# Optimization experiments

Measured on AMD Instinct MI355X. Metric: run time of the kernel, lower is better.

## Reference

```python
import jax, jax.numpy as jnp
import numpy as np

B, L, H, NH, DH = 2, 4096, 768, 12, 64
W_ = 128          # one-sided sliding window
NL = 2            # encoder layers
VOCAB, OUT, FF = 50265, 384, 3072
EPS = 1e-5


def _ln(x, s, b):
    m = jnp.mean(x, axis=-1, keepdims=True)
    v = jnp.mean((x - m) ** 2, axis=-1, keepdims=True)
    return (x - m) / jnp.sqrt(v + EPS) * s + b


def _attn(x, amask, Wq, bq, Wk, bk, Wv, bv, Wo, bo):
    # x: [B,L,H]; sliding-window attention (one-sided W_) + global token 0
    def heads(Wt, bt):
        return (x @ Wt + bt).reshape(B, L, NH, DH).transpose(0, 2, 1, 3)  # [B,NH,L,DH]
    q, k, v = heads(Wq, bq), heads(Wk, bk), heads(Wv, bv)
    scale = 1.0 / np.sqrt(DH).astype(np.float32)
    C = W_
    nC = L // C
    qc = q.reshape(B, NH, nC, C, DH)

    def blocks(t):  # gather [prev, self, next] key chunks -> [B,NH,nC,3C,DH]
        tc = t.reshape(B, NH, nC, C, DH)
        tp = jnp.pad(tc, ((0, 0), (0, 0), (1, 1), (0, 0), (0, 0)))
        return jnp.concatenate([tp[:, :, :-2], tp[:, :, 1:-1], tp[:, :, 2:]], axis=3)

    k3, v3 = blocks(k), blocks(v)
    s_loc = jnp.einsum('bhncd,bhnkd->bhnck', qc, k3) * scale  # [B,NH,nC,C,3C]

    pos_k = (jnp.arange(nC)[:, None] - 1) * C + jnp.arange(3 * C)[None, :]  # [nC,3C]
    pos_q = jnp.arange(nC)[:, None] * C + jnp.arange(C)[None, :]            # [nC,C]
    within = jnp.abs(pos_q[:, :, None] - pos_k[:, None, :]) <= W_           # [nC,C,3C]
    valid = (pos_k >= 0) & (pos_k < L) & (pos_k != 0)  # key 0 handled as global column
    mk = amask[:, jnp.clip(pos_k, 0, L - 1)] > 0        # [B,nC,3C]
    m = within[None, None] & valid[None, None, :, None, :] & mk[:, None, :, None, :]
    s_loc = jnp.where(m, s_loc, -1e9)

    # every token also attends to the global token 0
    s_g = jnp.einsum('bhld,bhd->bhl', q, k[:, :, 0]) * scale  # [B,NH,L]
    s = jnp.concatenate([s_loc.reshape(B, NH, L, 3 * C), s_g[..., None]], axis=-1)
    p = jax.nn.softmax(s, axis=-1)
    p_loc = p[..., :3 * C].reshape(B, NH, nC, C, 3 * C)
    out = jnp.einsum('bhnck,bhnkd->bhncd', p_loc, v3).reshape(B, NH, L, DH)
    out = out + p[..., -1:] * v[:, :, 0][:, :, None, :]

    # global token 0 attends to everything
    s0 = jnp.einsum('bhd,bhld->bhl', q[:, :, 0], k) * scale
    s0 = jnp.where(amask[:, None, :] > 0, s0, -1e9)
    o0 = jnp.einsum('bhl,bhld->bhd', jax.nn.softmax(s0, axis=-1), v)
    out = out.at[:, :, 0, :].set(o0)

    out = out.transpose(0, 2, 1, 3).reshape(B, L, H)
    return out @ Wo + bo


def setup_inputs() -> dict:
    key = jax.random.key(0)
    ks = jax.random.split(key, 16)
    p = lambda k_, sh: 0.02 * jax.random.normal(k_, sh, jnp.float32)
    return {
        'input_ids': jax.random.randint(ks[0], (B, L), 0, VOCAB, dtype=jnp.int32),
        'attention_mask': jnp.ones((B, L), jnp.int32),
        'word_emb': p(ks[1], (VOCAB, H)),
        'pos_emb': p(ks[2], (L, H)),
        'emb_ln_s': jnp.ones((H,), jnp.float32), 'emb_ln_b': jnp.zeros((H,), jnp.float32),
        'Wq': p(ks[3], (NL, H, H)), 'bq': jnp.zeros((NL, H), jnp.float32),
        'Wk': p(ks[4], (NL, H, H)), 'bk': jnp.zeros((NL, H), jnp.float32),
        'Wv': p(ks[5], (NL, H, H)), 'bv': jnp.zeros((NL, H), jnp.float32),
        'Wo': p(ks[6], (NL, H, H)), 'bo': jnp.zeros((NL, H), jnp.float32),
        'ln1_s': jnp.ones((NL, H), jnp.float32), 'ln1_b': jnp.zeros((NL, H), jnp.float32),
        'W1': p(ks[7], (NL, H, FF)), 'b1': jnp.zeros((NL, FF), jnp.float32),
        'W2': p(ks[8], (NL, FF, H)), 'b2': jnp.zeros((NL, H), jnp.float32),
        'ln2_s': jnp.ones((NL, H), jnp.float32), 'ln2_b': jnp.zeros((NL, H), jnp.float32),
        'Wfc': p(ks[9], (H, OUT)), 'bfc': jnp.zeros((OUT,), jnp.float32),
    }


def reference(input_ids, attention_mask, word_emb, pos_emb, emb_ln_s, emb_ln_b,
              Wq, bq, Wk, bk, Wv, bv, Wo, bo, ln1_s, ln1_b,
              W1, b1, W2, b2, ln2_s, ln2_b, Wfc, bfc):
    x = word_emb[input_ids] + pos_emb[None]
    x = _ln(x, emb_ln_s, emb_ln_b)
    for l in range(NL):
        a = _attn(x, attention_mask, Wq[l], bq[l], Wk[l], bk[l], Wv[l], bv[l], Wo[l], bo[l])
        x = _ln(x + a, ln1_s[l], ln1_b[l])
        h = jax.nn.gelu(x @ W1[l] + b1[l])
        x = _ln(x + h @ W2[l] + b2[l], ln2_s[l], ln2_b[l])
    v_dn = x @ Wfc + bfc           # [B,L,OUT]
    cls = v_dn[:, 0]               # fc(last_hidden[:,0]) == v_dn[:,0]
    return v_dn, cls
```

## Files before the change

kernel.cpp:

```cpp
#include <hip/hip_runtime.h>
#include <hip/hip_bf16.h>
#include <stdint.h>

#define L_SEQ 4096
#define H_DIM 768
#define N_HEADS 12
#define D_HEAD 64
#define N_CHUNK 32
#define CHUNK 128
#define FF_DIM 3072
#define OUT_DIM 384
#define BATCH 2
#define EPS_LN 1e-5f
#define M_ROWS (BATCH * L_SEQ)
#define QKV_LD (3 * H_DIM)
#define NSEG 16

typedef unsigned short u16;
typedef __bf16 bx8 __attribute__((ext_vector_type(8)));
typedef float fx4 __attribute__((ext_vector_type(4)));
typedef u16 ux8 __attribute__((ext_vector_type(8)));

__device__ __forceinline__ u16 f2bf(float f) {
  union { float f; unsigned u; } x; x.f = f;
  unsigned r = x.u + 0x7fffu + ((x.u >> 16) & 1u);
  return (u16)(r >> 16);
}
__device__ __forceinline__ float bf2f(u16 v) {
  union { unsigned u; float f; } x; x.u = ((unsigned)v) << 16;
  return x.f;
}

__device__ __forceinline__ void gload16(const void* g, void* l) {
  __builtin_amdgcn_global_load_lds((const __attribute__((address_space(1))) void*)g,
                                   (__attribute__((address_space(3))) void*)l, 16, 0, 0);
}

template<int OUT_BF16, int DO_GELU, int DO_CLS>
__global__ __launch_bounds__(256, 3)
void gemm_s(const u16* __restrict__ A, const u16* __restrict__ Bt,
            const float* __restrict__ bias,
            float* __restrict__ Cf, u16* __restrict__ Cb,
            float* __restrict__ cls,
            int N, int K)
{
  __shared__ __align__(16) u16 As[128 * 64];
  __shared__ __align__(16) u16 Bs[128 * 64];
  const int tid = threadIdx.x;
  const int lane = tid & 63, w = tid >> 6;
  const int c16 = lane & 15, g = lane >> 4;
  const int wr = w >> 1, wc = w & 1;

  const int nbn = N >> 7;
  int id = blockIdx.x;
  id = (id & 7) * (gridDim.x >> 3) + (id >> 3);
  const int bm = id / nbn, bn = id % nbn;

  const int srow = w * 8 + (lane >> 3);
  const int schunk = (lane & 7) ^ (lane >> 3);
  const u16* sA = A + (size_t)(bm * 128 + srow) * K + schunk * 8;
  const u16* sB = Bt + (size_t)(bn * 128 + srow) * K + schunk * 8;
  const int wdst = w * 512;

  fx4 acc[4][4] = {};

  for (int k0 = 0; k0 < K; k0 += 64) {
    #pragma unroll
    for (int i = 0; i < 4; i++) {
      gload16(sA + (size_t)(i * 32) * K + k0, &As[i * 2048 + wdst]);
      gload16(sB + (size_t)(i * 32) * K + k0, &Bs[i * 2048 + wdst]);
    }
    __syncthreads();
    #pragma unroll
    for (int h = 0; h < 2; h++) {
      bx8 af[4], bf[4];
      #pragma unroll
      for (int m = 0; m < 4; m++) {
        const int row = wr * 64 + m * 16 + c16;
        af[m] = *(const bx8*)&As[row * 64 + (((h << 2) + g) ^ (c16 & 7)) * 8];
      }
      #pragma unroll
      for (int n = 0; n < 4; n++) {
        const int row = wc * 64 + n * 16 + c16;
        bf[n] = *(const bx8*)&Bs[row * 64 + (((h << 2) + g) ^ (c16 & 7)) * 8];
      }
      #pragma unroll
      for (int m = 0; m < 4; m++)
        #pragma unroll
        for (int n = 0; n < 4; n++)
          acc[m][n] = __builtin_amdgcn_mfma_f32_16x16x32_bf16(af[m], bf[n], acc[m][n], 0, 0, 0);
    }
    __syncthreads();
  }

  const int row0 = bm * 128 + wr * 64 + g * 4;
  const int col0 = bn * 128 + wc * 64 + c16;
  #pragma unroll
  for (int n = 0; n < 4; n++) {
    const int col = col0 + n * 16;
    const float bb = bias[col];
    #pragma unroll
    for (int m = 0; m < 4; m++) {
      #pragma unroll
      for (int r = 0; r < 4; r++) {
        float y = acc[m][n][r] + bb;
        if (DO_GELU) {
          const float tt = y;
          y = 0.5f * tt * (1.0f + tanhf(0.7978845608f * (tt + 0.044715f * tt * tt * tt)));
        }
        const int row = row0 + m * 16 + r;
        const size_t idx = (size_t)row * N + col;
        if (OUT_BF16) Cb[idx] = f2bf(y);
        else Cf[idx] = y;
        if (DO_CLS) {
          if ((row & (L_SEQ - 1)) == 0)
            cls[(row >> 12) * OUT_DIM + col] = y;
        }
      }
    }
  }
}

#define KV_W 384
#define P_STR 128

__global__ __launch_bounds__(512, 2)
void attn_local_kernel(const u16* __restrict__ qkv, const int* __restrict__ amask,
                       u16* __restrict__ attnout)
{
  __shared__ __align__(16) u16 Klds[KV_W * 64];
  __shared__ __align__(16) u16 Vlds[64 * KV_W];
  __shared__ __align__(16) u16 Plds[8 * 16 * P_STR];

  const int tid = threadIdx.x;
  const int lane = tid & 63, w = tid >> 6;
  const int c16 = lane & 15, g = lane >> 4;

  const int bh = blockIdx.x >> 5;
  const int n = blockIdx.x & 31;
  const int b = bh / N_HEADS, h = bh % N_HEADS;

  const u16* qkvb = qkv + (size_t)b * L_SEQ * QKV_LD + h * D_HEAD;
  const int chunk_lo = n * CHUNK - CHUNK;

  #pragma unroll
  for (int it = 0; it < 6; it++) {
    const int row = it * 64 + w * 8 + (lane >> 3);
    const int sc = (lane & 7) ^ (row & 7);
    int pos = chunk_lo + row;
    if (pos < 0) pos = 0;
    if (pos >= L_SEQ) pos = L_SEQ - 1;
    gload16(qkvb + (size_t)pos * QKV_LD + H_DIM + sc * 8,
            &Klds[it * 4096 + w * 512]);
  }

  {
    const int d = lane;
    #pragma unroll
    for (int it = 0; it < 6; it++) {
      const int kb = it * 8 + w;
      ux8 vals;
      #pragma unroll
      for (int j = 0; j < 8; j++) {
        int pos = chunk_lo + kb * 8 + j;
        if (pos < 0) pos = 0;
        if (pos >= L_SEQ) pos = L_SEQ - 1;
        vals[j] = qkvb[(size_t)pos * QKV_LD + 2 * H_DIM + d];
      }
      *(ux8*)&Vlds[d * KV_W + ((kb ^ (d & 7)) << 3)] = vals;
    }
  }

  const int qrow = n * CHUNK + w * 16 + c16;
  const u16* qp = qkvb + (size_t)qrow * QKV_LD + g * 8;
  const bx8 aq0 = *(const bx8*)qp;
  const bx8 aq1 = *(const bx8*)(qp + 32);

  unsigned kvm = 0;
  #pragma unroll
  for (int kf = 0; kf < 24; kf++) {
    const int pos = chunk_lo + kf * 16 + c16;
    bool ok = (pos >= 1) && (pos < L_SEQ);
    if (ok) ok = (amask[b * L_SEQ + pos] > 0);
    kvm |= ((unsigned)ok) << kf;
  }

  const int cq = w * 16 + g * 4;

  float m[4], l[4], pgv[4];
  {
    const u16* kp = qkvb + H_DIM + g * 8;
    const bx8 b0 = *(const bx8*)kp;
    const bx8 b1 = *(const bx8*)(kp + 32);
    fx4 sg = {};
    sg = __builtin_amdgcn_mfma_f32_16x16x32_bf16(aq0, b0, sg, 0, 0, 0);
    sg = __builtin_amdgcn_mfma_f32_16x16x32_bf16(aq1, b1, sg, 0, 0, 0);
    #pragma unroll
    for (int r = 0; r < 4; r++) {
      const float val = (c16 == 0) ? sg[r] * 0.125f : -1.0e9f;
      float mm = val;
      mm = fmaxf(mm, __shfl_xor(mm, 1));
      mm = fmaxf(mm, __shfl_xor(mm, 2));
      mm = fmaxf(mm, __shfl_xor(mm, 4));
      mm = fmaxf(mm, __shfl_xor(mm, 8));
      m[r] = mm;
      pgv[r] = __expf(val - mm);
      float t = pgv[r];
      t += __shfl_xor(t, 1);
      t += __shfl_xor(t, 2);
      t += __shfl_xor(t, 4);
      t += __shfl_xor(t, 8);
      l[r] = t;
    }
  }

  __syncthreads();

  fx4 o[4] = {};
  u16* pb = Plds + w * 16 * P_STR;
  const int prow = (w * 16 + c16) * P_STR;

  #pragma unroll
  for (int pass = 0; pass < 4; pass++) {
    fx4 s[6];
    #pragma unroll
    for (int kf6 = 0; kf6 < 6; kf6++) {
      const int kf = pass * 6 + kf6;
      const int krow = kf * 16 + c16;
      const bx8 b0 = *(const bx8*)&Klds[krow * 64 + ((g ^ (c16 & 7)) << 3)];
      const bx8 b1 = *(const bx8*)&Klds[krow * 64 + (((4 + g) ^ (c16 & 7)) << 3)];
      fx4 a = {};
      a = __builtin_amdgcn_mfma_f32_16x16x32_bf16(aq0, b0, a, 0, 0, 0);
      a = __builtin_amdgcn_mfma_f32_16x16x32_bf16(aq1, b1, a, 0, 0, 0);
      s[kf6] = a;
    }
    float pmax[4];
    #pragma unroll
    for (int r = 0; r < 4; r++) pmax[r] = -3.0e38f;
    #pragma unroll
    for (int kf6 = 0; kf6 < 6; kf6++) {
      const int kf = pass * 6 + kf6;
      const int j = kf * 16 + c16;
      const bool kv = ((kvm >> kf) & 1u) != 0;
      #pragma unroll
      for (int r = 0; r < 4; r++) {
        const int c = cq + r;
        const bool keep = kv && (j >= c && j <= c + 256);
        const float val = keep ? s[kf6][r] * 0.125f : -1.0e9f;
        s[kf6][r] = val;
        pmax[r] = fmaxf(pmax[r], val);
      }
    }
    #pragma unroll
    for (int r = 0; r < 4; r++) {
      float mm = pmax[r];
      mm = fmaxf(mm, __shfl_xor(mm, 1));
      mm = fmaxf(mm, __shfl_xor(mm, 2));
      mm = fmaxf(mm, __shfl_xor(mm, 4));
      mm = fmaxf(mm, __shfl_xor(mm, 8));
      const float newm = fmaxf(m[r], mm);
      const float scale = __expf(m[r] - newm);
      m[r] = newm;
      l[r] *= scale;
      pgv[r] *= scale;
      #pragma unroll
      for (int df = 0; df < 4; df++) o[df][r] *= scale;
    }
    float lsum[4] = {0.f, 0.f, 0.f, 0.f};
    #pragma unroll
    for (int kf6 = 0; kf6 < 6; kf6++)
      #pragma unroll
      for (int r = 0; r < 4; r++) {
        const float p = __expf(s[kf6][r] - m[r]);
        s[kf6][r] = p;
        lsum[r] += p;
      }
    #pragma unroll
    for (int r = 0; r < 4; r++) {
      float t = lsum[r];
      t += __shfl_xor(t, 1);
      t += __shfl_xor(t, 2);
      t += __shfl_xor(t, 4);
      t += __shfl_xor(t, 8);
      l[r] += t;
    }
    #pragma unroll
    for (int kf6 = 0; kf6 < 6; kf6++) {
      #pragma unroll
      for (int r = 0; r < 4; r++) {
        const int rr = g * 4 + r;
        const int jj = kf6 * 16 + c16;
        pb[rr * P_STR + (((jj >> 3) ^ (rr & 7)) << 3) + (jj & 7)] = f2bf(s[kf6][r]);
      }
    }
    #pragma unroll
    for (int t = 0; t < 3; t++) {
      const int ckp = t * 4 + g;
      const bx8 pa = *(const bx8*)&Plds[prow + ((ckp ^ (c16 & 7)) << 3)];
      const int ckv = pass * 12 + ckp;
      #pragma unroll
      for (int df = 0; df < 4; df++) {
        const int vrow = df * 16 + c16;
        const bx8 vvf = *(const bx8*)&Vlds[vrow * KV_W + ((ckv ^ (c16 & 7)) << 3)];
        o[df] = __builtin_amdgcn_mfma_f32_16x16x32_bf16(pa, vvf, o[df], 0, 0, 0);
      }
    }
  }

  float rinv[4], pg[4];
  #pragma unroll
  for (int r = 0; r < 4; r++) {
    rinv[r] = 1.0f / l[r];
    pg[r] = __shfl(pgv[r], g * 16);
  }
  u16* ob = attnout + (size_t)b * L_SEQ * H_DIM + h * D_HEAD;
  const int posq = n * CHUNK + w * 16 + g * 4;
  #pragma unroll
  for (int df = 0; df < 4; df++) {
    const float v0f = bf2f(qkvb[2 * H_DIM + df * 16 + c16]);
    #pragma unroll
    for (int r = 0; r < 4; r++)
      ob[(size_t)(posq + r) * H_DIM + df * 16 + c16] =
          f2bf((o[df][r] + pg[r] * v0f) * rinv[r]);
  }
}

__global__ __launch_bounds__(256)
void attn_g_score(const u16* __restrict__ qkv, const int* __restrict__ amask,
                  float* __restrict__ sbuf, float* __restrict__ pmax)
{
  __shared__ float qs[D_HEAD];
  __shared__ float red[4];
  const int seg = blockIdx.x, bh = blockIdx.y;
  const int b = bh / N_HEADS, h = bh % N_HEADS;
  const u16* base = qkv + (size_t)b * L_SEQ * QKV_LD + h * D_HEAD;
  const int tid = threadIdx.x;

  if (tid < D_HEAD) qs[tid] = bf2f(base[tid]);
  __syncthreads();

  const int l = seg * 256 + tid;
  const ux8* kp = (const ux8*)(base + (size_t)l * QKV_LD + H_DIM);
  float dot = 0.f;
  #pragma unroll
  for (int i = 0; i < 8; i++) {
    const ux8 kv = kp[i];
    #pragma unroll
    for (int j = 0; j < 8; j++) dot += qs[i * 8 + j] * bf2f(kv[j]);
  }
  float sv = dot * 0.125f;
  if (amask[b * L_SEQ + l] == 0) sv = -1.0e9f;
  sbuf[(size_t)bh * L_SEQ + l] = sv;

  float m = sv;
  #pragma unroll
  for (int off = 32; off > 0; off >>= 1) m = fmaxf(m, __shfl_xor(m, off));
  if ((tid & 63) == 0) red[tid >> 6] = m;
  __syncthreads();
  if (tid == 0)
    pmax[bh * NSEG + seg] = fmaxf(fmaxf(red[0], red[1]), fmaxf(red[2], red[3]));
}

__global__ __launch_bounds__(256)
void attn_g_pv(const u16* __restrict__ qkv, const float* __restrict__ sbuf,
               const float* __restrict__ pmax, float* __restrict__ psum,
               float* __restrict__ po)
{
  __shared__ float es[256];
  __shared__ float red[4];
  const int seg = blockIdx.x, bh = blockIdx.y;
  const int b = bh / N_HEADS, h = bh % N_HEADS;
  const int tid = threadIdx.x;

  float M = -3.0e38f;
  #pragma unroll
  for (int i = 0; i < NSEG; i++) M = fmaxf(M, pmax[bh * NSEG + i]);

  const int l = seg * 256 + tid;
  const float e = __expf(sbuf[(size_t)bh * L_SEQ + l] - M);
  es[tid] = e;

  float t = e;
  #pragma unroll
  for (int off = 32; off > 0; off >>= 1) t += __shfl_xor(t, off);
  if ((tid & 63) == 0) red[tid >> 6] = t;
  __syncthreads();
  if (tid == 0) psum[bh * NSEG + seg] = red[0] + red[1] + red[2] + red[3];

  const int d = tid & 63, grp = tid >> 6;
  const u16* vb = qkv + (size_t)b * L_SEQ * QKV_LD + h * D_HEAD + 2 * H_DIM + d;
  float acc = 0.f;
  #pragma unroll 4
  for (int i = 0; i < 64; i++) {
    const int ll = seg * 256 + grp * 64 + i;
    acc += es[grp * 64 + i] * bf2f(vb[(size_t)ll * QKV_LD]);
  }
  po[(((size_t)bh * NSEG + seg) * 4 + grp) * D_HEAD + d] = acc;
}

__global__ __launch_bounds__(64)
void attn_g_combine(const float* __restrict__ psum, const float* __restrict__ po,
                    u16* __restrict__ attnout)
{
  const int bh = blockIdx.x;
  const int b = bh / N_HEADS, h = bh % N_HEADS;
  const int d = threadIdx.x;
  float S = 0.f;
  #pragma unroll
  for (int i = 0; i < NSEG; i++) S += psum[bh * NSEG + i];
  float acc = 0.f;
  #pragma unroll
  for (int i = 0; i < NSEG * 4; i++)
    acc += po[((size_t)bh * NSEG * 4 + i) * D_HEAD + d];
  attnout[(size_t)b * L_SEQ * H_DIM + h * D_HEAD + d] = f2bf(acc / S);
}

__device__ __forceinline__ void block_stats(float sum, float sq, float* red,
                                            float& mean, float& rstd)
{
  const int lane = threadIdx.x & 63, wv = threadIdx.x >> 6;
  #pragma unroll
  for (int off = 32; off > 0; off >>= 1) {
    sum += __shfl_xor(sum, off);
    sq  += __shfl_xor(sq, off);
  }
  if (lane == 0) { red[wv] = sum; red[4 + wv] = sq; }
  __syncthreads();
  sum = red[0] + red[1] + red[2] + red[3];
  sq  = red[4] + red[5] + red[6] + red[7];
  mean = sum * (1.0f / H_DIM);
  const float var = sq * (1.0f / H_DIM) - mean * mean;
  rstd = rsqrtf(var + EPS_LN);
}

__global__ __launch_bounds__(256)
void embed_ln_kernel(const int* __restrict__ ids, const float* __restrict__ wemb,
                     const float* __restrict__ pemb, const float* __restrict__ gam,
                     const float* __restrict__ bet, u16* __restrict__ xb)
{
  __shared__ float red[8];
  const int row = blockIdx.x, tid = threadIdx.x;
  const int l = row & (L_SEQ - 1);
  const int id = ids[row];
  float v[3]; float sum = 0.f, sq = 0.f;
  #pragma unroll
  for (int i = 0; i < 3; i++) {
    const int c = tid + i * 256;
    const float t = wemb[(size_t)id * H_DIM + c] + pemb[(size_t)l * H_DIM + c];
    v[i] = t; sum += t; sq += t * t;
  }
  float mean, rstd;
  block_stats(sum, sq, red, mean, rstd);
  #pragma unroll
  for (int i = 0; i < 3; i++) {
    const int c = tid + i * 256;
    const float y = (v[i] - mean) * rstd * gam[c] + bet[c];
    xb[(size_t)row * H_DIM + c] = f2bf(y);
  }
}

__global__ __launch_bounds__(256)
void add_ln_kernel(u16* xio, const u16* __restrict__ yin,
                   const float* __restrict__ gam, const float* __restrict__ bet)
{
  __shared__ float red[8];
  const int row = blockIdx.x, tid = threadIdx.x;
  float v[3]; float sum = 0.f, sq = 0.f;
  #pragma unroll
  for (int i = 0; i < 3; i++) {
    const int c = tid + i * 256;
    const float t = bf2f(xio[(size_t)row * H_DIM + c]) + bf2f(yin[(size_t)row * H_DIM + c]);
    v[i] = t; sum += t; sq += t * t;
  }
  float mean, rstd;
  block_stats(sum, sq, red, mean, rstd);
  #pragma unroll
  for (int i = 0; i < 3; i++) {
    const int c = tid + i * 256;
    const float y = (v[i] - mean) * rstd * gam[c] + bet[c];
    xio[(size_t)row * H_DIM + c] = f2bf(y);
  }
}

__global__ __launch_bounds__(256)
void prep_weights(const float* __restrict__ Wq, const float* __restrict__ Wk,
                  const float* __restrict__ Wv, const float* __restrict__ Wo,
                  const float* __restrict__ W1, const float* __restrict__ W2,
                  const float* __restrict__ Wfc,
                  const float* __restrict__ bq, const float* __restrict__ bk,
                  const float* __restrict__ bv,
                  u16* __restrict__ wqkvT, u16* __restrict__ woT,
                  u16* __restrict__ w1T, u16* __restrict__ w2T,
                  u16* __restrict__ wfcT, float* __restrict__ bqkv)
{
  const int t = blockIdx.x;
  const int tid = threadIdx.x;
  if (t >= 14112) {
    const int idx = t - 14112;
    const int l = idx / 9, j = idx % 9;
    const int i = j * 256 + tid;
    if (i < H_DIM)          bqkv[l * QKV_LD + i] = bq[l * H_DIM + i];
    else if (i < 2 * H_DIM) bqkv[l * QKV_LD + i] = bk[l * H_DIM + i - H_DIM];
    else if (i < 3 * H_DIM) bqkv[l * QKV_LD + i] = bv[l * H_DIM + i - 2 * H_DIM];
    return;
  }
  const float* src; u16* dst; int K, N, r;
  if (t < 13824) {
    const int l = t / 6912; r = t % 6912;
    if (r < 2304) {
      const int m = r / 576; r = r % 576; K = H_DIM; N = H_DIM;
      if (m == 0)      src = Wq + (size_t)l * H_DIM * H_DIM;
      else if (m == 1) src = Wk + (size_t)l * H_DIM * H_DIM;
      else if (m == 2) src = Wv + (size_t)l * H_DIM * H_DIM;
      else             src = Wo + (size_t)l * H_DIM * H_DIM;
      dst = (m < 3) ? wqkvT + (size_t)l * QKV_LD * H_DIM + (size_t)m * H_DIM * H_DIM
                    : woT + (size_t)l * H_DIM * H_DIM;
    } else if (r < 4608) {
      r -= 2304; K = H_DIM; N = FF_DIM;
      src = W1 + (size_t)l * H_DIM * FF_DIM;
      dst = w1T + (size_t)l * FF_DIM * H_DIM;
    } else {
      r -= 4608; K = FF_DIM; N = H_DIM;
      src = W2 + (size_t)l * FF_DIM * H_DIM;
      dst = w2T + (size_t)l * H_DIM * FF_DIM;
    }
  } else {
    r = t - 13824; K = H_DIM; N = OUT_DIM; src = Wfc; dst = wfcT;
  }
  const int ntn = N >> 5;
  const int k0 = (r / ntn) * 32, n0 = (r % ntn) * 32;
  __shared__ float tile[32][33];
  const int tx = tid & 31, ty = tid >> 5;
  #pragma unroll
  for (int i = 0; i < 32; i += 8)
    tile[ty + i][tx] = src[(size_t)(k0 + ty + i) * N + n0 + tx];
  __syncthreads();
  #pragma unroll
  for (int i = 0; i < 32; i += 8)
    dst[(size_t)(n0 + ty + i) * K + k0 + tx] = f2bf(tile[tx][ty + i]);
}

extern "C" void kernel_launch(void* const* d_in, const int* in_sizes, int n_in,
                              void* d_out, int out_size, void* d_ws, size_t ws_size,
                              hipStream_t stream)
{
  (void)in_sizes; (void)n_in; (void)out_size; (void)ws_size;
  const int*   ids   = (const int*)d_in[0];
  const int*   amask = (const int*)d_in[1];
  const float* wemb  = (const float*)d_in[2];
  const float* pemb  = (const float*)d_in[3];
  const float* elns  = (const float*)d_in[4];
  const float* elnb  = (const float*)d_in[5];
  const float* Wq    = (const float*)d_in[6];
  const float* bq    = (const float*)d_in[7];
  const float* Wk    = (const float*)d_in[8];
  const float* bk    = (const float*)d_in[9];
  const float* Wv    = (const float*)d_in[10];
  const float* bv    = (const float*)d_in[11];
  const float* Wo    = (const float*)d_in[12];
  const float* bo    = (const float*)d_in[13];
  const float* ln1s  = (const float*)d_in[14];
  const float* ln1b  = (const float*)d_in[15];
  const float* W1    = (const float*)d_in[16];
  const float* b1    = (const float*)d_in[17];
  const float* W2    = (const float*)d_in[18];
  const float* b2    = (const float*)d_in[19];
  const float* ln2s  = (const float*)d_in[20];
  const float* ln2b  = (const float*)d_in[21];
  const float* Wfc   = (const float*)d_in[22];
  const float* bfc   = (const float*)d_in[23];

  char* ws = (char*)d_ws;
  size_t off = 0;
  auto alloc = [&](size_t bytes) -> void* {
    void* p = ws + off;
    off += (bytes + 255) & ~(size_t)255;
    return p;
  };
  u16* xb     = (u16*)alloc((size_t)M_ROWS * H_DIM * 2);
  u16* projb  = (u16*)alloc((size_t)M_ROWS * H_DIM * 2);
  u16* big    = (u16*)alloc((size_t)M_ROWS * FF_DIM * 2);
  u16* attno  = (u16*)alloc((size_t)M_ROWS * H_DIM * 2);
  u16* wqkvT  = (u16*)alloc((size_t)2 * QKV_LD * H_DIM * 2);
  u16* woT    = (u16*)alloc((size_t)2 * H_DIM * H_DIM * 2);
  u16* w1T    = (u16*)alloc((size_t)2 * FF_DIM * H_DIM * 2);
  u16* w2T    = (u16*)alloc((size_t)2 * H_DIM * FF_DIM * 2);
  u16* wfcT   = (u16*)alloc((size_t)OUT_DIM * H_DIM * 2);
  float* bqkv = (float*)alloc(2 * QKV_LD * 4);
  float* gsc  = (float*)alloc((size_t)BATCH * N_HEADS * L_SEQ * 4);
  float* gpm  = (float*)alloc((size_t)BATCH * N_HEADS * NSEG * 4);
  float* gps  = (float*)alloc((size_t)BATCH * N_HEADS * NSEG * 4);
  float* gpo  = (float*)alloc((size_t)BATCH * N_HEADS * NSEG * 4 * D_HEAD * 4);

  u16* qkvb = big;
  u16* ff1  = big;

  prep_weights<<<14130, 256, 0, stream>>>(Wq, Wk, Wv, Wo, W1, W2, Wfc,
                                          bq, bk, bv,
                                          wqkvT, woT, w1T, w2T, wfcT, bqkv);
  embed_ln_kernel<<<M_ROWS, 256, 0, stream>>>(ids, wemb, pemb, elns, elnb, xb);

  for (int l = 0; l < 2; l++) {
    gemm_s<1, 0, 0><<<(M_ROWS / 128) * (QKV_LD / 128), 256, 0, stream>>>(
        xb, wqkvT + (size_t)l * QKV_LD * H_DIM, bqkv + l * QKV_LD,
        nullptr, qkvb, nullptr, QKV_LD, H_DIM);
    attn_local_kernel<<<BATCH * N_HEADS * N_CHUNK, 512, 0, stream>>>(qkvb, amask, attno);
    attn_g_score<<<dim3(NSEG, BATCH * N_HEADS), 256, 0, stream>>>(qkvb, amask, gsc, gpm);
    attn_g_pv<<<dim3(NSEG, BATCH * N_HEADS), 256, 0, stream>>>(qkvb, gsc, gpm, gps, gpo);
    attn_g_combine<<<BATCH * N_HEADS, 64, 0, stream>>>(gps, gpo, attno);
    gemm_s<1, 0, 0><<<(M_ROWS / 128) * (H_DIM / 128), 256, 0, stream>>>(
        attno, woT + (size_t)l * H_DIM * H_DIM, bo + l * H_DIM,
        nullptr, projb, nullptr, H_DIM, H_DIM);
    add_ln_kernel<<<M_ROWS, 256, 0, stream>>>(xb, projb, ln1s + l * H_DIM, ln1b + l * H_DIM);
    gemm_s<1, 1, 0><<<(M_ROWS / 128) * (FF_DIM / 128), 256, 0, stream>>>(
        xb, w1T + (size_t)l * FF_DIM * H_DIM, b1 + l * FF_DIM,
        nullptr, ff1, nullptr, FF_DIM, H_DIM);
    gemm_s<1, 0, 0><<<(M_ROWS / 128) * (H_DIM / 128), 256, 0, stream>>>(
        ff1, w2T + (size_t)l * H_DIM * FF_DIM, b2 + l * H_DIM,
        nullptr, projb, nullptr, H_DIM, FF_DIM);
    add_ln_kernel<<<M_ROWS, 256, 0, stream>>>(xb, projb, ln2s + l * H_DIM, ln2b + l * H_DIM);
  }

  float* vdn = (float*)d_out;
  float* cls = vdn + (size_t)BATCH * L_SEQ * OUT_DIM;
  gemm_s<0, 0, 1><<<(M_ROWS / 128) * (OUT_DIM / 128), 256, 0, stream>>>(
      xb, wfcT, bfc, vdn, nullptr, cls, OUT_DIM, H_DIM);
}
```

Baseline: 575.9 us.

## Stream K/V through LDS in 64-key tiles to cut attention shared memory

The local attention kernel used to load the whole 384-key K and V window into LDS up front, about 112KB including the P buffer. It now loops over six 64-key tiles and reloads K and V into small 8KB buffers each iteration, with the P staging stride halved. This shrinks LDS per block so the requested two blocks per CU can actually be resident. The cost is two extra __syncthreads per tile and no overlap between the global loads and the MFMA work.

```diff
diff --git a/kernel.cpp b/kernel.cpp
--- a/kernel.cpp
+++ b/kernel.cpp
@@ -121,16 +121,15 @@
   }
 }
 
-#define KV_W 384
-#define P_STR 128
+#define P2_STR 64
 
 __global__ __launch_bounds__(512, 2)
 void attn_local_kernel(const u16* __restrict__ qkv, const int* __restrict__ amask,
                        u16* __restrict__ attnout)
 {
-  __shared__ __align__(16) u16 Klds[KV_W * 64];
-  __shared__ __align__(16) u16 Vlds[64 * KV_W];
-  __shared__ __align__(16) u16 Plds[8 * 16 * P_STR];
+  __shared__ __align__(16) u16 Klds[64 * 64];
+  __shared__ __align__(16) u16 Vlds[64 * 64];
+  __shared__ __align__(16) u16 Plds[8 * 16 * P2_STR];
 
   const int tid = threadIdx.x;
   const int lane = tid & 63, w = tid >> 6;
@@ -142,34 +141,6 @@
 
   const u16* qkvb = qkv + (size_t)b * L_SEQ * QKV_LD + h * D_HEAD;
   const int chunk_lo = n * CHUNK - CHUNK;
-
-  #pragma unroll
-  for (int it = 0; it < 6; it++) {
-    const int row = it * 64 + w * 8 + (lane >> 3);
-    const int sc = (lane & 7) ^ (row & 7);
-    int pos = chunk_lo + row;
-    if (pos < 0) pos = 0;
-    if (pos >= L_SEQ) pos = L_SEQ - 1;
-    gload16(qkvb + (size_t)pos * QKV_LD + H_DIM + sc * 8,
-            &Klds[it * 4096 + w * 512]);
-  }
-
-  {
-    const int d = lane;
-    #pragma unroll
-    for (int it = 0; it < 6; it++) {
-      const int kb = it * 8 + w;
-      ux8 vals;
-      #pragma unroll
-      for (int j = 0; j < 8; j++) {
-        int pos = chunk_lo + kb * 8 + j;
-        if (pos < 0) pos = 0;
-        if (pos >= L_SEQ) pos = L_SEQ - 1;
-        vals[j] = qkvb[(size_t)pos * QKV_LD + 2 * H_DIM + d];
-      }
-      *(ux8*)&Vlds[d * KV_W + ((kb ^ (d & 7)) << 3)] = vals;
-    }
-  }
 
   const int qrow = n * CHUNK + w * 16 + c16;
   const u16* qp = qkvb + (size_t)qrow * QKV_LD + g * 8;
@@ -214,40 +185,60 @@
     }
   }
 
-  __syncthreads();
-
   fx4 o[4] = {};
-  u16* pb = Plds + w * 16 * P_STR;
-  const int prow = (w * 16 + c16) * P_STR;
-
-  #pragma unroll
-  for (int pass = 0; pass < 4; pass++) {
-    fx4 s[6];
-    #pragma unroll
-    for (int kf6 = 0; kf6 < 6; kf6++) {
-      const int kf = pass * 6 + kf6;
+  u16* pb = Plds + w * 16 * P2_STR;
+  const int prow = (w * 16 + c16) * P2_STR;
+
+  for (int t = 0; t < 6; t++) {
+    if (t) __syncthreads();
+
+    {
+      const int row = w * 8 + (lane >> 3);
+      const int sc = (lane & 7) ^ (row & 7);
+      int pos = chunk_lo + t * 64 + row;
+      if (pos < 0) pos = 0;
+      if (pos >= L_SEQ) pos = L_SEQ - 1;
+      gload16(qkvb + (size_t)pos * QKV_LD + H_DIM + sc * 8, &Klds[w * 512]);
+    }
+    {
+      const int d = lane;
+      ux8 vals;
+      #pragma unroll
+      for (int j = 0; j < 8; j++) {
+        int pos = chunk_lo + t * 64 + w * 8 + j;
+        if (pos < 0) pos = 0;
+        if (pos >= L_SEQ) pos = L_SEQ - 1;
+        vals[j] = qkvb[(size_t)pos * QKV_LD + 2 * H_DIM + d];
+      }
+      *(ux8*)&Vlds[d * 64 + ((w ^ (d & 7)) << 3)] = vals;
+    }
+    __syncthreads();
+
+    fx4 s[4];
+    #pragma unroll
+    for (int kf = 0; kf < 4; kf++) {
       const int krow = kf * 16 + c16;
       const bx8 b0 = *(const bx8*)&Klds[krow * 64 + ((g ^ (c16 & 7)) << 3)];
       const bx8 b1 = *(const bx8*)&Klds[krow * 64 + (((4 + g) ^ (c16 & 7)) << 3)];
       fx4 a = {};
       a = __builtin_amdgcn_mfma_f32_16x16x32_bf16(aq0, b0, a, 0, 0, 0);
       a = __builtin_amdgcn_mfma_f32_16x16x32_bf16(aq1, b1, a, 0, 0, 0);
-      s[kf6] = a;
+      s[kf] = a;
     }
     float pmax[4];
     #pragma unroll
     for (int r = 0; r < 4; r++) pmax[r] = -3.0e38f;
     #pragma unroll
-    for (int kf6 = 0; kf6 < 6; kf6++) {
-      const int kf = pass * 6 + kf6;
-      const int j = kf * 16 + c16;
-      const bool kv = ((kvm >> kf) & 1u) != 0;
+    for (int kf = 0; kf < 4; kf++) {
+      const int KF = t * 4 + kf;
+      const int j = KF * 16 + c16;
+      const bool kv = ((kvm >> KF) & 1u) != 0;
       #pragma unroll
       for (int r = 0; r < 4; r++) {
         const int c = cq + r;
         const bool keep = kv && (j >= c && j <= c + 256);
-        const float val = keep ? s[kf6][r] * 0.125f : -1.0e9f;
-        s[kf6][r] = val;
+        const float val = keep ? s[kf][r] * 0.125f : -1.0e9f;
+        s[kf][r] = val;
         pmax[r] = fmaxf(pmax[r], val);
       }
     }
@@ -268,40 +259,39 @@
     }
     float lsum[4] = {0.f, 0.f, 0.f, 0.f};
     #pragma unroll
-    for (int kf6 = 0; kf6 < 6; kf6++)
+    for (int kf = 0; kf < 4; kf++)
       #pragma unroll
       for (int r = 0; r < 4; r++) {
-        const float p = __expf(s[kf6][r] - m[r]);
-        s[kf6][r] = p;
+        const float p = __expf(s[kf][r] - m[r]);
+        s[kf][r] = p;
         lsum[r] += p;
       }
     #pragma unroll
     for (int r = 0; r < 4; r++) {
-      float t = lsum[r];
-      t += __shfl_xor(t, 1);
-      t += __shfl_xor(t, 2);
-      t += __shfl_xor(t, 4);
-      t += __shfl_xor(t, 8);
-      l[r] += t;
-    }
-    #pragma unroll
-    for (int kf6 = 0; kf6 < 6; kf6++) {
+      float tt = lsum[r];
+      tt += __shfl_xor(tt, 1);
+      tt += __shfl_xor(tt, 2);
+      tt += __shfl_xor(tt, 4);
+      tt += __shfl_xor(tt, 8);
+      l[r] += tt;
+    }
+    #pragma unroll
+    for (int kf = 0; kf < 4; kf++) {
       #pragma unroll
       for (int r = 0; r < 4; r++) {
         const int rr = g * 4 + r;
-        const int jj = kf6 * 16 + c16;
-        pb[rr * P_STR + (((jj >> 3) ^ (rr & 7)) << 3) + (jj & 7)] = f2bf(s[kf6][r]);
-      }
-    }
-    #pragma unroll
-    for (int t = 0; t < 3; t++) {
-      const int ckp = t * 4 + g;
+        const int jj = kf * 16 + c16;
+        pb[rr * P2_STR + (((jj >> 3) ^ (rr & 7)) << 3) + (jj & 7)] = f2bf(s[kf][r]);
+      }
+    }
+    #pragma unroll
+    for (int kt = 0; kt < 2; kt++) {
+      const int ckp = kt * 4 + g;
       const bx8 pa = *(const bx8*)&Plds[prow + ((ckp ^ (c16 & 7)) << 3)];
-      const int ckv = pass * 12 + ckp;
       #pragma unroll
       for (int df = 0; df < 4; df++) {
         const int vrow = df * 16 + c16;
-        const bx8 vvf = *(const bx8*)&Vlds[vrow * KV_W + ((ckv ^ (c16 & 7)) << 3)];
+        const bx8 vvf = *(const bx8*)&Vlds[vrow * 64 + ((ckp ^ (c16 & 7)) << 3)];
         o[df] = __builtin_amdgcn_mfma_f32_16x16x32_bf16(pa, vvf, o[df], 0, 0, 0);
       }
     }
```

Measured after the change: 557.3 us. 1.03x faster.
